# Optimization experiments

Hardware: AMD Instinct MI355X
Metric: run time of the kernel (lower is better)

Reference implementation:

```python
import jax, jax.numpy as jnp
import numpy as np

NUM_CODES = 100000
DIM = 64
N_VISITS = 16384
MAX_CODES = 64


def setup_inputs() -> dict:
    key = jax.random.key(0)
    k1, k2 = jax.random.split(key)
    # ids in [-5, NUM_CODES): negatives act as padding (original filters ids >= 0)
    code_ids = jax.random.randint(k1, (N_VISITS, MAX_CODES), -5, NUM_CODES, dtype=jnp.int64)
    emb_weight = jax.random.normal(k2, (NUM_CODES, DIM), dtype=jnp.float32)
    return {"code_ids": code_ids, "emb_weight": emb_weight}


def reference(code_ids, emb_weight):
    # mask of valid (non-negative) code ids per visit
    mask = code_ids >= 0                                  # [N, C] bool
    safe_ids = jnp.where(mask, code_ids, 0)               # clamp padding to 0 for gather
    x = emb_weight[safe_ids]                              # [N, C, D] gather
    maskf = mask.astype(emb_weight.dtype)
    sums = jnp.einsum('ncd,nc->nd', x, maskf)             # masked sum over codes
    counts = maskf.sum(axis=1, keepdims=True)             # [N, 1]
    # mean over valid ids; visits with zero valid ids -> zero vector
    out = sums / jnp.maximum(counts, 1.0)
    return jnp.where(counts > 0, out, 0.0)
```

## Files before the change

### kernel.cpp

```cpp
#include <hip/hip_runtime.h>
#include <hip/hip_fp16.h>

#define N_VISITS  16384
#define MAX_CODES 64
#define DIM       64
#define NUM_CODES 100000
#define NRANGES   2
#define RANGE_SIZE 50000

typedef float f32x4 __attribute__((ext_vector_type(4)));
typedef float f32x2 __attribute__((ext_vector_type(2)));

__global__ __launch_bounds__(256) void emb_to_half_kernel(
    const float* __restrict__ emb, __half* __restrict__ embh)
{
    const size_t i = (size_t)blockIdx.x * 256 + threadIdx.x;
    const f32x4* src = (const f32x4*)emb + 2 * i;
    f32x4 a = __builtin_nontemporal_load(src);
    f32x4 b = __builtin_nontemporal_load(src + 1);
    union { __half2 h[4]; f32x4 f; } u;
    u.h[0] = __floats2half2_rn(a.x, a.y);
    u.h[1] = __floats2half2_rn(a.z, a.w);
    u.h[2] = __floats2half2_rn(b.x, b.y);
    u.h[3] = __floats2half2_rn(b.z, b.w);
    ((f32x4*)embh)[i] = u.f;
}

__global__ __launch_bounds__(256) void gather2_partial_kernel(
    const int* __restrict__ code_ids,
    const __half* __restrict__ embh,
    float* __restrict__ partials)
{
    __shared__ int slots[4][64];

    const int w    = threadIdx.x >> 6;
    const int lane = threadIdx.x & 63;
    const int p    = blockIdx.x & 1;
    const int g    = blockIdx.x >> 1;
    const int visit = g * 4 + w;
    const int lo = p * RANGE_SIZE;
    const int hi = lo + RANGE_SIZE;

    const int r = lane >> 4;
    const int t = lane & 15;

    const int my_id = __builtin_nontemporal_load(
        code_ids + (size_t)visit * MAX_CODES + lane);

    const unsigned long long vmask = __ballot(my_id >= 0);
    const int total = __popcll(vmask);

    const bool inr = (my_id >= lo) && (my_id < hi);
    const unsigned long long rmask = __ballot(inr);
    const int nrows = __popcll(rmask);
    const int rank  = __popcll(rmask & ((1ull << lane) - 1ull));
    if (inr) slots[w][rank] = my_id;

    const int ngather = (nrows + 3) >> 2;

    float acc[4] = {0.f, 0.f, 0.f, 0.f};
    for (int j = 0; j < ngather; ++j) {
        const int s = 4 * j + r;
        if (s < nrows) {
            const int id = slots[w][s];
            union { f32x2 f; __half2 h[2]; } u;
            u.f = *(const f32x2*)(embh + (size_t)id * DIM + t * 4);
            const float2 f0 = __half22float2(u.h[0]);
            const float2 f1 = __half22float2(u.h[1]);
            acc[0] += f0.x; acc[1] += f0.y;
            acc[2] += f1.x; acc[3] += f1.y;
        }
    }

    #pragma unroll
    for (int k = 0; k < 4; ++k) acc[k] += __shfl_xor(acc[k], 16, 64);
    #pragma unroll
    for (int k = 0; k < 4; ++k) acc[k] += __shfl_xor(acc[k], 32, 64);

    if (lane < 16) {
        const float scale = (total > 0) ? (1.0f / (float)total) : 0.0f;
        f32x4 o;
        o.x = acc[0] * scale; o.y = acc[1] * scale;
        o.z = acc[2] * scale; o.w = acc[3] * scale;
        f32x4* dst = (f32x4*)(partials + ((size_t)visit * NRANGES + p) * DIM + t * 4);
        __builtin_nontemporal_store(o, dst);
    }
}

__global__ __launch_bounds__(256) void reduce2_kernel(
    const float* __restrict__ partials, float* __restrict__ out)
{
    const int i = blockIdx.x * 256 + threadIdx.x;
    const int visit = i >> 4;
    const int c     = i & 15;
    const f32x4* base = (const f32x4*)partials + (size_t)visit * 32 + c;
    f32x4 s0 = __builtin_nontemporal_load(base);
    f32x4 s1 = __builtin_nontemporal_load(base + 16);
    s0.x += s1.x; s0.y += s1.y; s0.z += s1.z; s0.w += s1.w;
    __builtin_nontemporal_store(s0, (f32x4*)out + i);
}

extern "C" void kernel_launch(void* const* d_in, const int* in_sizes, int n_in,
                              void* d_out, int out_size, void* d_ws, size_t ws_size,
                              hipStream_t stream) {
    const int*   code_ids = (const int*)d_in[0];
    const float* emb      = (const float*)d_in[1];
    float*       out      = (float*)d_out;

    __half* embh     = (__half*)d_ws;
    float*  partials = (float*)((char*)d_ws + (16u << 20));

    emb_to_half_kernel<<<3125, 256, 0, stream>>>(emb, embh);

    gather2_partial_kernel<<<8192, 256, 0, stream>>>(code_ids, embh, partials);

    reduce2_kernel<<<1024, 256, 0, stream>>>(partials, out);
}
```

Baseline: 106.1 us.

## Split embedding table into eight XCD-local slices with fp16 partials

Partitions the fp16 embedding table into eight row slices and assigns them by blockIdx&7, so each XCD's L2 holds only its own slice for both the conversion and the gather kernels. The gather now launches 8 blocks per visit group, each summing only the ids that fall in its slice. Partial sums are stored as fp16 and reduced over eight slices. The aim is a better L2 hit rate on the random gathers. In exchange it quadruples the gather launch, with each wave doing far less work and repeating the id load and ballot, adds partial traffic, and rounds the partials to fp16.

```diff
diff --git a/kernel.cpp b/kernel.cpp
--- a/kernel.cpp
+++ b/kernel.cpp
@@ -1,45 +1,55 @@
 #include <hip/hip_runtime.h>
 #include <hip/hip_fp16.h>
 
-#define N_VISITS  16384
-#define MAX_CODES 64
-#define DIM       64
-#define NUM_CODES 100000
-#define NRANGES   2
-#define RANGE_SIZE 50000
+#define N_VISITS   16384
+#define MAX_CODES  64
+#define DIM        64
+#define NUM_CODES  100000
+#define NSLICES    8
+#define SLICE_ROWS 12500
+#define SLICE_F4   100000
+#define PER_BLK    391
 
 typedef float f32x4 __attribute__((ext_vector_type(4)));
 typedef float f32x2 __attribute__((ext_vector_type(2)));
 
-__global__ __launch_bounds__(256) void emb_to_half_kernel(
+__global__ __launch_bounds__(256) void emb_to_half_xcd_kernel(
     const float* __restrict__ emb, __half* __restrict__ embh)
 {
-    const size_t i = (size_t)blockIdx.x * 256 + threadIdx.x;
-    const f32x4* src = (const f32x4*)emb + 2 * i;
-    f32x4 a = __builtin_nontemporal_load(src);
-    f32x4 b = __builtin_nontemporal_load(src + 1);
-    union { __half2 h[4]; f32x4 f; } u;
-    u.h[0] = __floats2half2_rn(a.x, a.y);
-    u.h[1] = __floats2half2_rn(a.z, a.w);
-    u.h[2] = __floats2half2_rn(b.x, b.y);
-    u.h[3] = __floats2half2_rn(b.z, b.w);
-    ((f32x4*)embh)[i] = u.f;
+    const int s = blockIdx.x & 7;
+    const int q = blockIdx.x >> 3;
+    #pragma unroll
+    for (int it = 0; it < 2; ++it) {
+        const int local = (int)threadIdx.x + it * 256;
+        if (local >= PER_BLK) break;
+        const int k = q * PER_BLK + local;
+        if (k >= SLICE_F4) break;
+        const f32x4* src = (const f32x4*)emb + (size_t)s * (2 * SLICE_F4) + 2 * (size_t)k;
+        f32x4 a = __builtin_nontemporal_load(src);
+        f32x4 b = __builtin_nontemporal_load(src + 1);
+        union { __half2 h[4]; f32x4 f; } u;
+        u.h[0] = __floats2half2_rn(a.x, a.y);
+        u.h[1] = __floats2half2_rn(a.z, a.w);
+        u.h[2] = __floats2half2_rn(b.x, b.y);
+        u.h[3] = __floats2half2_rn(b.z, b.w);
+        ((f32x4*)embh)[(size_t)s * SLICE_F4 + k] = u.f;
+    }
 }
 
-__global__ __launch_bounds__(256) void gather2_partial_kernel(
+__global__ __launch_bounds__(256) void gather8_partial_kernel(
     const int* __restrict__ code_ids,
     const __half* __restrict__ embh,
-    float* __restrict__ partials)
+    __half* __restrict__ partials)
 {
     __shared__ int slots[4][64];
 
     const int w    = threadIdx.x >> 6;
     const int lane = threadIdx.x & 63;
-    const int p    = blockIdx.x & 1;
-    const int g    = blockIdx.x >> 1;
+    const int p    = blockIdx.x & 7;
+    const int g    = blockIdx.x >> 3;
     const int visit = g * 4 + w;
-    const int lo = p * RANGE_SIZE;
-    const int hi = lo + RANGE_SIZE;
+    const int lo = p * SLICE_ROWS;
+    const int hi = lo + SLICE_ROWS;
 
     const int r = lane >> 4;
     const int t = lane & 15;
@@ -60,9 +70,9 @@
 
     float acc[4] = {0.f, 0.f, 0.f, 0.f};
     for (int j = 0; j < ngather; ++j) {
-        const int s = 4 * j + r;
-        if (s < nrows) {
-            const int id = slots[w][s];
+        const int sidx = 4 * j + r;
+        if (sidx < nrows) {
+            const int id = slots[w][sidx];
             union { f32x2 f; __half2 h[2]; } u;
             u.f = *(const f32x2*)(embh + (size_t)id * DIM + t * 4);
             const float2 f0 = __half22float2(u.h[0]);
@@ -79,25 +89,33 @@
 
     if (lane < 16) {
         const float scale = (total > 0) ? (1.0f / (float)total) : 0.0f;
-        f32x4 o;
-        o.x = acc[0] * scale; o.y = acc[1] * scale;
-        o.z = acc[2] * scale; o.w = acc[3] * scale;
-        f32x4* dst = (f32x4*)(partials + ((size_t)visit * NRANGES + p) * DIM + t * 4);
-        __builtin_nontemporal_store(o, dst);
+        union { __half2 h[2]; f32x2 f; } o;
+        o.h[0] = __floats2half2_rn(acc[0] * scale, acc[1] * scale);
+        o.h[1] = __floats2half2_rn(acc[2] * scale, acc[3] * scale);
+        __builtin_nontemporal_store(
+            o.f, (f32x2*)(partials + ((size_t)visit * NSLICES + p) * DIM) + t);
     }
 }
 
-__global__ __launch_bounds__(256) void reduce2_kernel(
-    const float* __restrict__ partials, float* __restrict__ out)
+__global__ __launch_bounds__(256) void reduce8_kernel(
+    const __half* __restrict__ partials, float* __restrict__ out)
 {
     const int i = blockIdx.x * 256 + threadIdx.x;
     const int visit = i >> 4;
     const int c     = i & 15;
-    const f32x4* base = (const f32x4*)partials + (size_t)visit * 32 + c;
-    f32x4 s0 = __builtin_nontemporal_load(base);
-    f32x4 s1 = __builtin_nontemporal_load(base + 16);
-    s0.x += s1.x; s0.y += s1.y; s0.z += s1.z; s0.w += s1.w;
-    __builtin_nontemporal_store(s0, (f32x4*)out + i);
+
+    const __half* base = partials + (size_t)visit * NSLICES * DIM + c * 4;
+    float a0 = 0.f, a1 = 0.f, a2 = 0.f, a3 = 0.f;
+    #pragma unroll
+    for (int p = 0; p < NSLICES; ++p) {
+        union { f32x2 f; __half2 h[2]; } u;
+        u.f = __builtin_nontemporal_load((const f32x2*)(base + (size_t)p * DIM));
+        const float2 f0 = __half22float2(u.h[0]);
+        const float2 f1 = __half22float2(u.h[1]);
+        a0 += f0.x; a1 += f0.y; a2 += f1.x; a3 += f1.y;
+    }
+    f32x4 o; o.x = a0; o.y = a1; o.z = a2; o.w = a3;
+    __builtin_nontemporal_store(o, (f32x4*)out + i);
 }
 
 extern "C" void kernel_launch(void* const* d_in, const int* in_sizes, int n_in,
@@ -107,12 +125,12 @@
     const float* emb      = (const float*)d_in[1];
     float*       out      = (float*)d_out;
 
-    __half* embh     = (__half*)d_ws;
-    float*  partials = (float*)((char*)d_ws + (16u << 20));
+    __half* embh = (__half*)d_ws;
+    __half* ph   = (__half*)((char*)d_ws + (16u << 20));
 
-    emb_to_half_kernel<<<3125, 256, 0, stream>>>(emb, embh);
+    emb_to_half_xcd_kernel<<<2048, 256, 0, stream>>>(emb, embh);
 
-    gather2_partial_kernel<<<8192, 256, 0, stream>>>(code_ids, embh, partials);
+    gather8_partial_kernel<<<32768, 256, 0, stream>>>(code_ids, embh, ph);
 
-    reduce2_kernel<<<1024, 256, 0, stream>>>(partials, out);
+    reduce8_kernel<<<1024, 256, 0, stream>>>(ph, out);
 }
```

Result: slower. 130.0 us (+22.6%).
